# Kernel optimization log

Hardware: AMD Instinct MI355X
Metric: run time of the kernel (lower is better)

The kernel has to match this reference:

```python
import jax, jax.numpy as jnp
import numpy as np

N, E, B, K = 100000, 3200000, 500, 30
F_IN, H1, NUM_CLASSES = 128, 64, 18


def _gcn_conv(x, W, b, row, col, w_edge, n_nodes):
    # PyG GCNConv: remove_self_loops happened outside (w_edge=0 on self loops),
    # GCNConv re-adds self loops -> deg = in_deg + 1, norm = d^-1/2[row]*d^-1/2[col].
    xw = x @ W
    deg = jax.ops.segment_sum(w_edge, col, num_segments=n_nodes) + 1.0
    dis = jax.lax.rsqrt(deg)
    coef = dis[row] * dis[col] * w_edge           # [E]
    msg = xw[row] * coef[:, None]                 # [E, C] irregular gather
    agg = jax.ops.segment_sum(msg, col, num_segments=n_nodes)
    agg = agg + xw * (dis * dis)[:, None]         # self-loop term
    return agg + b


def _sort_pool(x, batch, num_graphs, k):
    # SortAggregation: per-graph sort descending by last channel, keep top-k, zero-pad.
    n, c = x.shape
    score = x[:, -1]
    perm = jnp.lexsort((-score, batch))           # sort by (batch asc, score desc)
    b_sorted = batch[perm]
    counts = jax.ops.segment_sum(jnp.ones((n,), x.dtype), batch, num_segments=num_graphs)
    starts = jnp.cumsum(counts) - counts          # segment start offsets
    pos = jnp.arange(n) - starts[b_sorted].astype(jnp.int32)
    pos = jnp.where(pos < k, pos, k)              # out-of-range -> dropped
    out = jnp.zeros((num_graphs, k, c), x.dtype).at[b_sorted, pos].set(x[perm], mode='drop')
    return out.reshape(num_graphs, k * c)


def _conv1d(x, w, b, stride):
    y = jax.lax.conv_general_dilated(x, w, (stride,), 'VALID',
                                     dimension_numbers=('NCH', 'OIH', 'NCH'))
    return y + b[None, :, None]


def setup_inputs() -> dict:
    key = jax.random.key(0)
    ks = jax.random.split(key, 16)
    x = jax.random.normal(ks[0], (N, F_IN), dtype=jnp.float32)
    edge_index = jax.random.randint(ks[1], (2, E), 0, N, dtype=jnp.int32)
    batch = jnp.sort(jax.random.randint(ks[2], (N,), 0, B, dtype=jnp.int32))
    s = 0.05
    return {
        'x': x, 'edge_index': edge_index, 'batch': batch, 'num_graphs': B,
        'W1': jax.random.normal(ks[3], (F_IN, H1), jnp.float32) * s,
        'b1': jnp.zeros((H1,), jnp.float32),
        'W2': jax.random.normal(ks[4], (H1, 1), jnp.float32) * s,
        'b2': jnp.zeros((1,), jnp.float32),
        'conv3_w': jax.random.normal(ks[5], (16, 1, 97), jnp.float32) * s,
        'conv3_b': jnp.zeros((16,), jnp.float32),
        'conv4_w': jax.random.normal(ks[6], (32, 16, 5), jnp.float32) * s,
        'conv4_b': jnp.zeros((32,), jnp.float32),
        'fc1_w': jax.random.normal(ks[7], (192, 128), jnp.float32) * s,
        'fc1_b': jnp.zeros((128,), jnp.float32),
        'fc2_w': jax.random.normal(ks[8], (128, NUM_CLASSES), jnp.float32) * s,
        'fc2_b': jnp.zeros((NUM_CLASSES,), jnp.float32),
    }


def reference(x, edge_index, batch, num_graphs, W1, b1, W2, b2,
              conv3_w, conv3_b, conv4_w, conv4_b, fc1_w, fc1_b, fc2_w, fc2_b):
    row, col = edge_index[0], edge_index[1]
    w_edge = (row != col).astype(x.dtype)         # remove_self_loops
    x1 = jnp.tanh(_gcn_conv(x, W1, b1, row, col, w_edge, x.shape[0]))   # [N,64]
    x2 = jnp.tanh(_gcn_conv(x1, W2, b2, row, col, w_edge, x.shape[0]))  # [N,1]
    xc = jnp.concatenate([x1, x2], axis=-1)       # [N,65]
    p = _sort_pool(xc, batch, num_graphs, K)      # [B, 1950]
    h = p[:, None, :]                             # [B,1,1950]
    h = jax.nn.relu(_conv1d(h, conv3_w, conv3_b, 97))                   # [B,16,20]
    h = jax.lax.reduce_window(h, -jnp.inf, jax.lax.max,
                              (1, 1, 2), (1, 1, 2), 'VALID')            # [B,16,10]
    h = jax.nn.relu(_conv1d(h, conv4_w, conv4_b, 1))                    # [B,32,6]
    h = h.reshape(h.shape[0], -1)                 # [B,192]
    last_layer = jax.nn.relu(h @ fc1_w + fc1_b)   # [B,128] (dropout = eval identity)
    out = last_layer @ fc2_w + fc2_b              # [B,18]
    classes = jax.nn.log_softmax(out, axis=-1)
    return (classes, out, last_layer)
```

## Files before the change

kernel.cpp:

```cpp
#include <hip/hip_runtime.h>
#include <math.h>

#define N_NODES 100000
#define N_EDGES 3200000
#define B_GRAPHS 500
#define K_TOP 30
#define F_INN 128
#define H1C 64
#define NUM_CLASSES 18
#define XC 65
#define P_LEN (K_TOP * XC)
#define C3_OUT 16
#define C3_K 97
#define C3_L 20
#define P2_L 10
#define C4_OUT 32
#define C4_K 5
#define C4_L 6
#define FC1_IN 192
#define FC1_OUT 128

#define BK_SHIFT 7
#define BK_NODES 128
#define NBKT ((N_NODES + BK_NODES - 1) / BK_NODES)
#define BSTRIDE 5120
#define MS_EPT 32
#define MS_EPB (256 * MS_EPT)

#define REG_B 544

typedef __attribute__((ext_vector_type(8))) short bf16x8;
typedef __attribute__((ext_vector_type(4))) float f32x4;
typedef __attribute__((ext_vector_type(2))) unsigned int u32x2;

static __device__ __forceinline__ unsigned short f2bf(float f) {
    unsigned int u = __float_as_uint(f);
    u += 0x7FFFu + ((u >> 16) & 1u);
    return (unsigned short)(u >> 16);
}

__global__ __launch_bounds__(256) void k_mscatter(const int* __restrict__ row,
                                                  const int* __restrict__ col,
                                                  int* __restrict__ gcur,
                                                  unsigned int* __restrict__ ebkt) {
    __shared__ int hist[NBKT];
    __shared__ int base[NBKT];
    int tid = threadIdx.x;
    for (int i = tid; i < NBKT; i += 256) hist[i] = 0;
    __syncthreads();
    unsigned int pk[MS_EPT];
    unsigned int pay[MS_EPT];
    int e0 = blockIdx.x * MS_EPB;
#pragma unroll
    for (int j = 0; j < MS_EPT; ++j) {
        int e = e0 + j * 256 + tid;
        pk[j] = 0xFFFFFFFFu;
        if (e < N_EDGES) {
            int r = row[e], c = col[e];
            if (r != c) {
                int b = c >> BK_SHIFT;
                int rank = atomicAdd(&hist[b], 1);
                pk[j] = ((unsigned int)b << 12) | (unsigned int)rank;
                pay[j] = ((unsigned int)r << BK_SHIFT) | (unsigned int)(c & (BK_NODES - 1));
            }
        }
    }
    __syncthreads();
    for (int i = tid; i < NBKT; i += 256)
        base[i] = hist[i] ? (i * BSTRIDE + atomicAdd(&gcur[i], hist[i])) : 0;
    __syncthreads();
#pragma unroll
    for (int j = 0; j < MS_EPT; ++j) {
        if (pk[j] != 0xFFFFFFFFu) {
            int b = pk[j] >> 12;
            int rank = pk[j] & 0xFFF;
            ebkt[base[b] + rank] = pay[j];
        }
    }
}

__global__ __launch_bounds__(256) void k_csr(const unsigned int* __restrict__ ebkt,
                                             const int* __restrict__ gcur,
                                             float* __restrict__ dis,
                                             int2* __restrict__ rowse,
                                             int* __restrict__ erow) {
    __shared__ unsigned int ebs[BSTRIDE];
    __shared__ int cnt[BK_NODES];
    __shared__ int s[256];
    __shared__ int cur[BK_NODES];
    int b = blockIdx.x, t = threadIdx.x;
    if (t < BK_NODES) cnt[t] = 0;
    __syncthreads();
    int n = gcur[b];
    int lo = b * BSTRIDE;
    for (int i = t; i < n; i += 256) {
        unsigned int pk = ebkt[lo + i];
        ebs[i] = pk;
        atomicAdd(&cnt[pk & (BK_NODES - 1)], 1);
    }
    __syncthreads();
    int v = (t < BK_NODES) ? cnt[t] : 0;
    s[t] = v;
    __syncthreads();
    for (int off = 1; off < BK_NODES; off <<= 1) {
        int add = (t >= off) ? s[t - off] : 0;
        __syncthreads();
        s[t] += add;
        __syncthreads();
    }
    int ex = s[t] - v;
    if (t < BK_NODES) {
        int node = b * BK_NODES + t;
        if (node < N_NODES) {
            dis[node] = rsqrtf((float)v + 1.0f);
            rowse[node] = make_int2(lo + ex, lo + ex + v);
        }
        cur[t] = lo + ex;
    }
    __syncthreads();
    for (int i = t; i < n; i += 256) {
        unsigned int pk = ebs[i];
        int cl = pk & (BK_NODES - 1);
        int slot = atomicAdd(&cur[cl], 1);
        erow[slot] = (int)((pk >> BK_SHIFT) << 7);
    }
}

__global__ __launch_bounds__(256) void k_xw1(const float* __restrict__ x,
                                             const float* __restrict__ W1,
                                             const float* __restrict__ dis,
                                             unsigned short* __restrict__ xw) {
    __shared__ unsigned short w1s[16 * 64 * 8];
    int tid = threadIdx.x;
    if (blockIdx.x == 0 && tid < 32)
        ((unsigned int*)(xw + (size_t)N_NODES * H1C))[tid] = 0;
    for (int idx = tid; idx < 16 * 64 * 8; idx += 256) {
        int f = idx >> 9;
        int l = (idx >> 3) & 63;
        int j = idx & 7;
        int kq = f >> 2, t4 = f & 3;
        int k = kq * 32 + ((l >> 4) << 3) + j;
        int n = t4 * 16 + (l & 15);
        w1s[idx] = f2bf(W1[k * H1C + n]);
    }
    __syncthreads();
    int wave = tid >> 6;
    int lane = tid & 63;
    int quad = lane >> 4;
    int m = lane & 15;
    int wrow0 = blockIdx.x * 256 + wave * 64;

    bf16x8 bw[16];
#pragma unroll
    for (int f = 0; f < 16; ++f)
        bw[f] = *(const bf16x8*)&w1s[(f * 64 + lane) * 8];

#pragma unroll
    for (int rt = 0; rt < 4; ++rt) {
        int trow0 = wrow0 + rt * 16;
        f32x4 acc[4];
#pragma unroll
        for (int t = 0; t < 4; ++t) acc[t] = (f32x4){0.f, 0.f, 0.f, 0.f};

        int rowA = trow0 + m;
        size_t ra = (size_t)(rowA < N_NODES ? rowA : N_NODES - 1);
#pragma unroll
        for (int kq = 0; kq < 4; ++kq) {
            const float* xp = x + ra * F_INN + kq * 32 + quad * 8;
            float4 f0 = ((const float4*)xp)[0];
            float4 f1 = ((const float4*)xp)[1];
            bf16x8 a;
            a[0] = (short)f2bf(f0.x); a[1] = (short)f2bf(f0.y);
            a[2] = (short)f2bf(f0.z); a[3] = (short)f2bf(f0.w);
            a[4] = (short)f2bf(f1.x); a[5] = (short)f2bf(f1.y);
            a[6] = (short)f2bf(f1.z); a[7] = (short)f2bf(f1.w);
#pragma unroll
            for (int t = 0; t < 4; ++t)
                acc[t] = __builtin_amdgcn_mfma_f32_16x16x32_bf16(a, bw[kq * 4 + t], acc[t], 0, 0, 0);
        }
#pragma unroll
        for (int r = 0; r < 4; ++r) {
            int rowD = trow0 + quad * 4 + r;
            if (rowD < N_NODES) {
                float dsc = dis[rowD];
#pragma unroll
                for (int t = 0; t < 4; ++t)
                    xw[(size_t)rowD * H1C + t * 16 + m] = f2bf(acc[t][r] * dsc);
            }
        }
    }
}

__global__ __launch_bounds__(256) void k_agg1m(const int2* __restrict__ rowse,
                                               const int* __restrict__ erow,
                                               const unsigned short* __restrict__ xws,
                                               const float* __restrict__ dis,
                                               const float* __restrict__ b1,
                                               const float* __restrict__ W2,
                                               float* __restrict__ x1,
                                               float* __restrict__ xws2) {
    __shared__ __align__(16) char slds[4][8 * REG_B];
    int tid = threadIdx.x;
    int wave = tid >> 6;
    int lane = tid & 63;
    int wid = blockIdx.x * 4 + wave;
    int grp = lane >> 3;
    int sub = lane & 7;
    int2 se = rowse[wid];
    int base = se.x, endp = se.y;
    int nE = endp - base;
    const char* xb = (const char*)xws;
    const int ZR = N_NODES << 7;

    char* wreg = &slds[wave][0];
    char* dst0 = wreg + ((sub >> 1) * 2 + ((grp >> 2) & 1)) * REG_B + (grp & 3) * 32 + (sub & 1) * 16;
    unsigned int trb = (unsigned int)(size_t)wreg +
                       (unsigned int)(((lane >> 4) * 64 + (lane & 15)) * 2);

    bf16x8 aones;
#pragma unroll
    for (int i = 0; i < 8; ++i) aones[i] = (short)0x3F80;

    f32x4 ac0 = (f32x4){0.f, 0.f, 0.f, 0.f};
    f32x4 ac1 = ac0, ac2 = ac0, ac3 = ac0;

    for (int w0 = 0; w0 < nE; w0 += 64) {
        int idx = base + w0 + lane;
        int myoff = (idx < endp) ? erow[idx] : ZR;
#pragma unroll
        for (int hf = 0; hf < 2; ++hf) {
            if (w0 + hf * 32 < nE) {
#pragma unroll
                for (int ii = 0; ii < 4; ++ii) {
                    int o = __shfl(myoff, hf * 32 + ii * 8 + grp);
                    uint4 v = ((const uint4*)(xb + o))[sub];
                    *(uint4*)(dst0 + ii * 128) = v;
                }
                asm volatile("s_waitcnt lgkmcnt(0)" ::: "memory");
                __builtin_amdgcn_sched_barrier(0);
                u32x2 q0, q1, q2, q3, q4, q5, q6, q7;
                asm volatile("ds_read_b64_tr_b16 %0, %1 offset:0"    : "=v"(q0) : "v"(trb) : "memory");
                asm volatile("ds_read_b64_tr_b16 %0, %1 offset:544"  : "=v"(q1) : "v"(trb) : "memory");
                asm volatile("ds_read_b64_tr_b16 %0, %1 offset:1088" : "=v"(q2) : "v"(trb) : "memory");
                asm volatile("ds_read_b64_tr_b16 %0, %1 offset:1632" : "=v"(q3) : "v"(trb) : "memory");
                asm volatile("ds_read_b64_tr_b16 %0, %1 offset:2176" : "=v"(q4) : "v"(trb) : "memory");
                asm volatile("ds_read_b64_tr_b16 %0, %1 offset:2720" : "=v"(q5) : "v"(trb) : "memory");
                asm volatile("ds_read_b64_tr_b16 %0, %1 offset:3264" : "=v"(q6) : "v"(trb) : "memory");
                asm volatile("ds_read_b64_tr_b16 %0, %1 offset:3808" : "=v"(q7) : "v"(trb) : "memory");
                asm volatile("s_waitcnt lgkmcnt(0)" ::: "memory");
                __builtin_amdgcn_sched_barrier(0);
                union FU { bf16x8 f; unsigned int d[4]; };
                FU f0, f1, f2, f3;
                f0.d[0] = q0.x; f0.d[1] = q0.y; f0.d[2] = q1.x; f0.d[3] = q1.y;
                f1.d[0] = q2.x; f1.d[1] = q2.y; f1.d[2] = q3.x; f1.d[3] = q3.y;
                f2.d[0] = q4.x; f2.d[1] = q4.y; f2.d[2] = q5.x; f2.d[3] = q5.y;
                f3.d[0] = q6.x; f3.d[1] = q6.y; f3.d[2] = q7.x; f3.d[3] = q7.y;
                ac0 = __builtin_amdgcn_mfma_f32_16x16x32_bf16(aones, f0.f, ac0, 0, 0, 0);
                ac1 = __builtin_amdgcn_mfma_f32_16x16x32_bf16(aones, f1.f, ac1, 0, 0, 0);
                ac2 = __builtin_amdgcn_mfma_f32_16x16x32_bf16(aones, f2.f, ac2, 0, 0, 0);
                ac3 = __builtin_amdgcn_mfma_f32_16x16x32_bf16(aones, f3.f, ac3, 0, 0, 0);
            }
        }
    }
    float v0 = __shfl(ac0[0], lane & 15);
    float v1 = __shfl(ac1[0], lane & 15);
    float v2 = __shfl(ac2[0], lane & 15);
    float v3 = __shfl(ac3[0], lane & 15);
    int ts = lane >> 4;
    float aggv = ts == 0 ? v0 : (ts == 1 ? v1 : (ts == 2 ? v2 : v3));
    float d = dis[wid];
    unsigned int su = xws[(size_t)wid * H1C + lane];
    float self = __uint_as_float(su << 16);
    float v = tanhf(d * (aggv + self) + b1[lane]);
    x1[(size_t)wid * H1C + lane] = v;
    float s = v * W2[lane];
#pragma unroll
    for (int off = 1; off < 64; off <<= 1) s += __shfl_xor(s, off);
    if (lane == 0) xws2[wid] = d * s;
}

__global__ __launch_bounds__(256) void k_x2(const int2* __restrict__ rowse,
                                            const int* __restrict__ erow,
                                            const float* __restrict__ xws2,
                                            const float* __restrict__ dis,
                                            const float* __restrict__ b2,
                                            float* __restrict__ x2) {
    int lane = threadIdx.x & 63;
    int wglob = (blockIdx.x * 256 + threadIdx.x) >> 6;
    int grp = lane >> 3;
    int sub = lane & 7;
    int node = wglob * 8 + grp;
    int2 se = rowse[node];
    float acc = 0.0f;
    for (int i = se.x + sub; i < se.y; i += 8)
        acc += xws2[erow[i] >> 7];
    acc += __shfl_xor(acc, 1);
    acc += __shfl_xor(acc, 2);
    acc += __shfl_xor(acc, 4);
    if (sub == 0)
        x2[node] = tanhf(dis[node] * (acc + xws2[node]) + b2[0]);
}

__global__ __launch_bounds__(256) void k_poolhead(const int* __restrict__ batch,
                                                  const float* __restrict__ x1,
                                                  const float* __restrict__ x2,
                                                  const float* __restrict__ w3, const float* __restrict__ b3,
                                                  const float* __restrict__ w4, const float* __restrict__ b4,
                                                  const float* __restrict__ fw1, const float* __restrict__ fb1,
                                                  const float* __restrict__ fw2, const float* __restrict__ fb2,
                                                  float* __restrict__ out) {
    __shared__ float x2s[512];
    __shared__ int sel[K_TOP];
    __shared__ float ps[P_LEN];
    __shared__ float h1s[C3_OUT * C3_L];
    __shared__ float h2s[C3_OUT * P2_L];
    __shared__ float h3s[FC1_IN];
    __shared__ float lls[FC1_OUT];
    __shared__ float outs[NUM_CLASSES];
    int g = blockIdx.x, tid = threadIdx.x;
    int lo = 0, hi = N_NODES;
    while (lo < hi) { int m = (lo + hi) >> 1; if (batch[m] < g) lo = m + 1; else hi = m; }
    int start = lo;
    hi = N_NODES;
    while (lo < hi) { int m = (lo + hi) >> 1; if (batch[m] < g + 1) lo = m + 1; else hi = m; }
    int end = lo;
    int count = end - start;
    if (count > 512) count = 512;
    for (int t = tid; t < count; t += 256) x2s[t] = x2[start + t];
    __syncthreads();
    int wave = tid >> 6, lane = tid & 63;
    if (wave == 0) {
        unsigned long long k[8];
#pragma unroll
        for (int i = 0; i < 8; ++i) {
            int idx = i * 64 + lane;
            unsigned long long key = 0ULL;
            if (idx < count) {
                unsigned int bits = __float_as_uint(x2s[idx]);
                unsigned int u = (bits & 0x80000000u) ? ~bits : (bits | 0x80000000u);
                key = ((unsigned long long)u << 32) | (unsigned int)(~(unsigned int)(start + idx));
            }
            k[i] = key;
        }
        int kk = count < K_TOP ? count : K_TOP;
        for (int j = 0; j < kk; ++j) {
            unsigned long long best = k[0];
#pragma unroll
            for (int i = 1; i < 8; ++i) if (k[i] > best) best = k[i];
#pragma unroll
            for (int off = 32; off; off >>= 1) {
                unsigned long long o = __shfl_xor(best, off);
                if (o > best) best = o;
            }
            int node = (int)(~(unsigned int)(best & 0xFFFFFFFFULL));
#pragma unroll
            for (int i = 0; i < 8; ++i) if (k[i] == best) k[i] = 0ULL;
            if (lane == 0) sel[j] = node;
        }
        if (lane >= kk && lane < K_TOP) sel[lane] = -1;
    }
    __syncthreads();
    for (int t = tid; t < P_LEN; t += 256) {
        int j = t / XC, c = t - j * XC;
        int node = sel[j];
        float v = 0.0f;
        if (node >= 0) v = (c < H1C) ? x1[(size_t)node * H1C + c] : x2s[node - start];
        ps[t] = v;
    }
    __syncthreads();
    for (int o = tid; o < C3_OUT * C3_L; o += 256) {
        int oc = o / C3_L, pos = o % C3_L;
        float s = b3[oc];
        const float* w = w3 + oc * C3_K;
        int base = pos * C3_K;
        for (int k = 0; k < C3_K; ++k) s += ps[base + k] * w[k];
        h1s[o] = fmaxf(s, 0.0f);
    }
    __syncthreads();
    if (tid < C3_OUT * P2_L) {
        int oc = tid / P2_L, pos = tid % P2_L;
        h2s[tid] = fmaxf(h1s[oc * C3_L + 2 * pos], h1s[oc * C3_L + 2 * pos + 1]);
    }
    __syncthreads();
    if (tid < C4_OUT * C4_L) {
        int oc = tid / C4_L, pos = tid % C4_L;
        float s = b4[oc];
        for (int ic = 0; ic < C3_OUT; ++ic)
#pragma unroll
            for (int k = 0; k < C4_K; ++k)
                s += h2s[ic * P2_L + pos + k] * w4[oc * C3_OUT * C4_K + ic * C4_K + k];
        h3s[oc * C4_L + pos] = fmaxf(s, 0.0f);
    }
    __syncthreads();
    if (tid < FC1_OUT) {
        float s = fb1[tid];
        for (int i = 0; i < FC1_IN; ++i) s += h3s[i] * fw1[i * FC1_OUT + tid];
        float v = fmaxf(s, 0.0f);
        lls[tid] = v;
        out[2 * B_GRAPHS * NUM_CLASSES + (size_t)g * FC1_OUT + tid] = v;
    }
    __syncthreads();
    if (tid < NUM_CLASSES) {
        float s = fb2[tid];
        for (int j = 0; j < FC1_OUT; ++j) s += lls[j] * fw2[j * NUM_CLASSES + tid];
        outs[tid] = s;
        out[B_GRAPHS * NUM_CLASSES + (size_t)g * NUM_CLASSES + tid] = s;
    }
    __syncthreads();
    if (tid < NUM_CLASSES) {
        float m = -INFINITY;
        for (int k2 = 0; k2 < NUM_CLASSES; ++k2) m = fmaxf(m, outs[k2]);
        float se = 0.0f;
        for (int k2 = 0; k2 < NUM_CLASSES; ++k2) se += expf(outs[k2] - m);
        out[(size_t)g * NUM_CLASSES + tid] = outs[tid] - m - logf(se);
    }
}

extern "C" void kernel_launch(void* const* d_in, const int* in_sizes, int n_in,
                              void* d_out, int out_size, void* d_ws, size_t ws_size,
                              hipStream_t stream) {
    const float* x   = (const float*)d_in[0];
    const int*   ei  = (const int*)d_in[1];
    const int*   row = ei;
    const int*   col = ei + N_EDGES;
    const int*   bat = (const int*)d_in[2];
    const float* W1  = (const float*)d_in[4];
    const float* b1  = (const float*)d_in[5];
    const float* W2  = (const float*)d_in[6];
    const float* b2  = (const float*)d_in[7];
    const float* w3  = (const float*)d_in[8];
    const float* b3  = (const float*)d_in[9];
    const float* w4  = (const float*)d_in[10];
    const float* b4  = (const float*)d_in[11];
    const float* fw1 = (const float*)d_in[12];
    const float* fb1 = (const float*)d_in[13];
    const float* fw2 = (const float*)d_in[14];
    const float* fb2 = (const float*)d_in[15];

    char* wsb = (char*)d_ws;
    unsigned short* xws = (unsigned short*)wsb;       wsb += (size_t)(N_NODES + 1) * H1C * 2;
    float* x1     = (float*)wsb;                      wsb += (size_t)N_NODES * H1C * 4;
    int*   erow   = (int*)wsb;                        wsb += (size_t)NBKT * BSTRIDE * 4;
    unsigned int* ebkt = (unsigned int*)x1;
    int*   gcur   = (int*)wsb;                        wsb += (size_t)NBKT * 4;
    int2*  rowse  = (int2*)wsb;                       wsb += (size_t)N_NODES * 8;
    float* dis    = (float*)wsb;                      wsb += (size_t)N_NODES * 4;
    float* xws2   = (float*)wsb;                      wsb += (size_t)N_NODES * 4;
    float* x2     = (float*)wsb;                      wsb += (size_t)N_NODES * 4;
    float* outp   = (float*)d_out;

    hipMemsetAsync(gcur, 0, (size_t)NBKT * 4, stream);

    k_mscatter<<<(N_EDGES + MS_EPB - 1) / MS_EPB, 256, 0, stream>>>(row, col, gcur, ebkt);
    k_csr<<<NBKT, 256, 0, stream>>>(ebkt, gcur, dis, rowse, erow);
    k_xw1<<<(N_NODES + 255) / 256, 256, 0, stream>>>(x, W1, dis, xws);
    k_agg1m<<<N_NODES / 4, 256, 0, stream>>>(rowse, erow, xws, dis, b1, W2, x1, xws2);
    k_x2<<<N_NODES / (8 * 4), 256, 0, stream>>>(rowse, erow, xws2, dis, b2, x2);
    k_poolhead<<<B_GRAPHS, 256, 0, stream>>>(bat, x1, x2,
                                             w3, b3, w4, b4, fw1, fb1, fw2, fb2, outp);
}
```

Baseline: 317.8 us.

## Prefetch gathers in GCN aggregation, vectorize edge loads, shrink xw1 tiles

The aggregation kernel now software-pipelines its neighbour-row gathers: the next half-window's global loads are issued before the current window's LDS transpose and MFMA work, and the next chunk of edge indices is loaded one group early. This is meant to hide gather latency. The edge bucketing kernel loads row and col as int4 vectors instead of scalars. The x@W1 kernel handles 16 rows per wave instead of 64, launching 4x more blocks for occupancy, at the cost of repeating the per-block W1 staging into LDS.

New measurement: 314.6 us. Within noise of the previous version (-1.0%).

```diff
diff --git a/kernel.cpp b/kernel.cpp
--- a/kernel.cpp
+++ b/kernel.cpp
@@ -50,18 +50,24 @@
     __syncthreads();
     unsigned int pk[MS_EPT];
     unsigned int pay[MS_EPT];
-    int e0 = blockIdx.x * MS_EPB;
-#pragma unroll
-    for (int j = 0; j < MS_EPT; ++j) {
-        int e = e0 + j * 256 + tid;
-        pk[j] = 0xFFFFFFFFu;
-        if (e < N_EDGES) {
-            int r = row[e], c = col[e];
-            if (r != c) {
+    int e0q = blockIdx.x * (MS_EPB / 4);
+#pragma unroll
+    for (int j = 0; j < MS_EPT / 4; ++j) {
+        int q = e0q + j * 256 + tid;
+        bool ok = (q * 4) < N_EDGES;
+        int4 r4 = ok ? ((const int4*)row)[q] : make_int4(0, 0, 0, 0);
+        int4 c4 = ok ? ((const int4*)col)[q] : make_int4(0, 0, 0, 0);
+#pragma unroll
+        for (int k = 0; k < 4; ++k) {
+            int jj = j * 4 + k;
+            pk[jj] = 0xFFFFFFFFu;
+            int r = k == 0 ? r4.x : k == 1 ? r4.y : k == 2 ? r4.z : r4.w;
+            int c = k == 0 ? c4.x : k == 1 ? c4.y : k == 2 ? c4.z : c4.w;
+            if (ok && r != c) {
                 int b = c >> BK_SHIFT;
                 int rank = atomicAdd(&hist[b], 1);
-                pk[j] = ((unsigned int)b << 12) | (unsigned int)rank;
-                pay[j] = ((unsigned int)r << BK_SHIFT) | (unsigned int)(c & (BK_NODES - 1));
+                pk[jj] = ((unsigned int)b << 12) | (unsigned int)rank;
+                pay[jj] = ((unsigned int)r << BK_SHIFT) | (unsigned int)(c & (BK_NODES - 1));
             }
         }
     }
@@ -148,45 +154,41 @@
     int lane = tid & 63;
     int quad = lane >> 4;
     int m = lane & 15;
-    int wrow0 = blockIdx.x * 256 + wave * 64;
+    int wrow0 = blockIdx.x * 64 + wave * 16;
 
     bf16x8 bw[16];
 #pragma unroll
     for (int f = 0; f < 16; ++f)
         bw[f] = *(const bf16x8*)&w1s[(f * 64 + lane) * 8];
 
-#pragma unroll
-    for (int rt = 0; rt < 4; ++rt) {
-        int trow0 = wrow0 + rt * 16;
-        f32x4 acc[4];
-#pragma unroll
-        for (int t = 0; t < 4; ++t) acc[t] = (f32x4){0.f, 0.f, 0.f, 0.f};
-
-        int rowA = trow0 + m;
-        size_t ra = (size_t)(rowA < N_NODES ? rowA : N_NODES - 1);
-#pragma unroll
-        for (int kq = 0; kq < 4; ++kq) {
-            const float* xp = x + ra * F_INN + kq * 32 + quad * 8;
-            float4 f0 = ((const float4*)xp)[0];
-            float4 f1 = ((const float4*)xp)[1];
-            bf16x8 a;
-            a[0] = (short)f2bf(f0.x); a[1] = (short)f2bf(f0.y);
-            a[2] = (short)f2bf(f0.z); a[3] = (short)f2bf(f0.w);
-            a[4] = (short)f2bf(f1.x); a[5] = (short)f2bf(f1.y);
-            a[6] = (short)f2bf(f1.z); a[7] = (short)f2bf(f1.w);
+    f32x4 acc[4];
+#pragma unroll
+    for (int t = 0; t < 4; ++t) acc[t] = (f32x4){0.f, 0.f, 0.f, 0.f};
+
+    int rowA = wrow0 + m;
+    size_t ra = (size_t)(rowA < N_NODES ? rowA : N_NODES - 1);
+#pragma unroll
+    for (int kq = 0; kq < 4; ++kq) {
+        const float* xp = x + ra * F_INN + kq * 32 + quad * 8;
+        float4 f0 = ((const float4*)xp)[0];
+        float4 f1 = ((const float4*)xp)[1];
+        bf16x8 a;
+        a[0] = (short)f2bf(f0.x); a[1] = (short)f2bf(f0.y);
+        a[2] = (short)f2bf(f0.z); a[3] = (short)f2bf(f0.w);
+        a[4] = (short)f2bf(f1.x); a[5] = (short)f2bf(f1.y);
+        a[6] = (short)f2bf(f1.z); a[7] = (short)f2bf(f1.w);
+#pragma unroll
+        for (int t = 0; t < 4; ++t)
+            acc[t] = __builtin_amdgcn_mfma_f32_16x16x32_bf16(a, bw[kq * 4 + t], acc[t], 0, 0, 0);
+    }
+#pragma unroll
+    for (int r = 0; r < 4; ++r) {
+        int rowD = wrow0 + quad * 4 + r;
+        if (rowD < N_NODES) {
+            float dsc = dis[rowD];
 #pragma unroll
             for (int t = 0; t < 4; ++t)
-                acc[t] = __builtin_amdgcn_mfma_f32_16x16x32_bf16(a, bw[kq * 4 + t], acc[t], 0, 0, 0);
-        }
-#pragma unroll
-        for (int r = 0; r < 4; ++r) {
-            int rowD = trow0 + quad * 4 + r;
-            if (rowD < N_NODES) {
-                float dsc = dis[rowD];
-#pragma unroll
-                for (int t = 0; t < 4; ++t)
-                    xw[(size_t)rowD * H1C + t * 16 + m] = f2bf(acc[t][r] * dsc);
-            }
+                xw[(size_t)rowD * H1C + t * 16 + m] = f2bf(acc[t][r] * dsc);
         }
     }
 }
@@ -224,17 +226,42 @@
     f32x4 ac0 = (f32x4){0.f, 0.f, 0.f, 0.f};
     f32x4 ac1 = ac0, ac2 = ac0, ac3 = ac0;
 
-    for (int w0 = 0; w0 < nE; w0 += 64) {
-        int idx = base + w0 + lane;
-        int myoff = (idx < endp) ? erow[idx] : ZR;
+    int nGroups = (nE + 63) >> 6;
+    int mo = ((base + lane) < endp) ? erow[base + lane] : ZR;
+    uint4 v0, v1, v2, v3;
+    if (nE > 0) {
+        int o0 = __shfl(mo, grp);
+        int o1 = __shfl(mo, 8 + grp);
+        int o2 = __shfl(mo, 16 + grp);
+        int o3 = __shfl(mo, 24 + grp);
+        v0 = ((const uint4*)(xb + o0))[sub];
+        v1 = ((const uint4*)(xb + o1))[sub];
+        v2 = ((const uint4*)(xb + o2))[sub];
+        v3 = ((const uint4*)(xb + o3))[sub];
+    }
+    for (int g = 0; g < nGroups; ++g) {
+        int idxn = base + (g + 1) * 64 + lane;
+        int mo_next = (idxn < endp) ? erow[idxn] : ZR;
 #pragma unroll
         for (int hf = 0; hf < 2; ++hf) {
-            if (w0 + hf * 32 < nE) {
-#pragma unroll
-                for (int ii = 0; ii < 4; ++ii) {
-                    int o = __shfl(myoff, hf * 32 + ii * 8 + grp);
-                    uint4 v = ((const uint4*)(xb + o))[sub];
-                    *(uint4*)(dst0 + ii * 128) = v;
+            int hw = g * 2 + hf;
+            if (hw * 32 < nE) {
+                *(uint4*)(dst0)       = v0;
+                *(uint4*)(dst0 + 128) = v1;
+                *(uint4*)(dst0 + 256) = v2;
+                *(uint4*)(dst0 + 384) = v3;
+                int nhw = hw + 1;
+                if (nhw * 32 < nE) {
+                    int moS = (nhw & 1) ? mo : mo_next;
+                    int off = (nhw & 1) << 5;
+                    int o0 = __shfl(moS, off + grp);
+                    int o1 = __shfl(moS, off + 8 + grp);
+                    int o2 = __shfl(moS, off + 16 + grp);
+                    int o3 = __shfl(moS, off + 24 + grp);
+                    v0 = ((const uint4*)(xb + o0))[sub];
+                    v1 = ((const uint4*)(xb + o1))[sub];
+                    v2 = ((const uint4*)(xb + o2))[sub];
+                    v3 = ((const uint4*)(xb + o3))[sub];
                 }
                 asm volatile("s_waitcnt lgkmcnt(0)" ::: "memory");
                 __builtin_amdgcn_sched_barrier(0);
@@ -261,13 +288,14 @@
                 ac3 = __builtin_amdgcn_mfma_f32_16x16x32_bf16(aones, f3.f, ac3, 0, 0, 0);
             }
         }
-    }
-    float v0 = __shfl(ac0[0], lane & 15);
-    float v1 = __shfl(ac1[0], lane & 15);
-    float v2 = __shfl(ac2[0], lane & 15);
-    float v3 = __shfl(ac3[0], lane & 15);
+        mo = mo_next;
+    }
+    float v0s = __shfl(ac0[0], lane & 15);
+    float v1s = __shfl(ac1[0], lane & 15);
+    float v2s = __shfl(ac2[0], lane & 15);
+    float v3s = __shfl(ac3[0], lane & 15);
     int ts = lane >> 4;
-    float aggv = ts == 0 ? v0 : (ts == 1 ? v1 : (ts == 2 ? v2 : v3));
+    float aggv = ts == 0 ? v0s : (ts == 1 ? v1s : (ts == 2 ? v2s : v3s));
     float d = dis[wid];
     unsigned int su = xws[(size_t)wid * H1C + lane];
     float self = __uint_as_float(su << 16);
@@ -453,7 +481,7 @@
 
     k_mscatter<<<(N_EDGES + MS_EPB - 1) / MS_EPB, 256, 0, stream>>>(row, col, gcur, ebkt);
     k_csr<<<NBKT, 256, 0, stream>>>(ebkt, gcur, dis, rowse, erow);
-    k_xw1<<<(N_NODES + 255) / 256, 256, 0, stream>>>(x, W1, dis, xws);
+    k_xw1<<<(N_NODES + 63) / 64, 256, 0, stream>>>(x, W1, dis, xws);
     k_agg1m<<<N_NODES / 4, 256, 0, stream>>>(rowse, erow, xws, dis, b1, W2, x1, xws2);
     k_x2<<<N_NODES / (8 * 4), 256, 0, stream>>>(rowse, erow, xws2, dis, b2, x2);
     k_poolhead<<<B_GRAPHS, 256, 0, stream>>>(bat, x1, x2,
```
